# Kernel tuning notes

Hardware: AMD Instinct MI355X
Metric: run time of the kernel (lower is better)

The kernel has to match this reference:

```python
import jax, jax.numpy as jnp
import numpy as np

B, T, C, H = 128, 512, 256, 64  # batch, seq (<= BLOCK_SIZE=512), EMBED_SIZE, HEAD_SIZE


def setup_inputs() -> dict:
    key = jax.random.key(0)
    k0, k1, k2, k3 = jax.random.split(key, 4)
    # nn.Linear(C, H, bias=False) applies x @ W.T with W:[H,C]; we store the
    # transposed weight [C,H] so the math x @ W is identical.
    scale = 1.0 / np.sqrt(C)  # rough Linear-init scale, values only matter for testing
    return {
        "input_embeddings": jax.random.normal(k0, (B, T, C), dtype=jnp.float32),
        "Wq": jax.random.normal(k1, (C, H), dtype=jnp.float32) * scale,
        "Wk": jax.random.normal(k2, (C, H), dtype=jnp.float32) * scale,
        "Wv": jax.random.normal(k3, (C, H), dtype=jnp.float32) * scale,
    }


def reference(input_embeddings, Wq, Wk, Wv):
    x = input_embeddings
    t = x.shape[1]
    h = Wq.shape[1]
    q = jnp.einsum("btc,ch->bth", x, Wq)
    k = jnp.einsum("btc,ch->bth", x, Wk)
    v = jnp.einsum("btc,ch->bth", x, Wv)
    # QK^T / sqrt(H), causal mask, softmax  (faithful to masked_fill(-inf))
    sim = jnp.einsum("bth,bsh->bts", q, k) / jnp.sqrt(jnp.asarray(h, x.dtype))
    causal = jnp.tril(jnp.ones((t, t), dtype=bool))
    sim = jnp.where(causal, sim, -jnp.inf)
    wei = jax.nn.softmax(sim, axis=-1)
    out = jnp.einsum("bts,bsh->bth", wei, v)
    return out
```

## Files before the change

### kernel.cpp

```cpp
#include <hip/hip_runtime.h>
#include <hip/hip_bf16.h>
#include <math.h>

#define Bn 128
#define Tn 512
#define Cn 256
#define Hn 64
#define HP2 72
#define SCL 0.18033688011112042f

typedef __attribute__((ext_vector_type(8))) short short8v;
typedef __attribute__((ext_vector_type(4))) float float4v;

__device__ __forceinline__ ushort f2bf(float f) {
    __hip_bfloat16 h = __float2bfloat16(f);
    return *reinterpret_cast<ushort*>(&h);
}

__global__ __launch_bounds__(256) void prep_w_kernel(
    const float* __restrict__ Wq, const float* __restrict__ Wk,
    const float* __restrict__ Wv, ushort* __restrict__ wcT4)
{
    const int g   = blockIdx.x;
    const int nh  = g / 96;
    const int row = g % 96;
    const int c   = threadIdx.x;
    const int kc  = c >> 6;
    const int k2  = c & 63;
    const float* W;
    int h;
    if (row < 64) { W = nh ? Wk : Wq; h = row; }
    else          { W = Wv; h = nh * 32 + (row - 64); }
    wcT4[(((nh * 4 + kc) * 96) + row) * 64 + (k2 ^ ((row & 7) << 3))] =
        f2bf(W[c * Hn + h]);
}

__global__ __launch_bounds__(256) void qkv_mfma_kernel(
    const float* __restrict__ x, const ushort* __restrict__ wcT4,
    ushort* __restrict__ q, ushort* __restrict__ k, ushort* __restrict__ vT)
{
    __shared__ char lds[40960];
    const int WOFF = 16384;

    const int tid  = threadIdx.x;
    const int lane = tid & 63;
    const int wv   = tid >> 6;
    const int lr   = lane & 15;
    const int hi   = lane >> 4;
    const int wr   = wv >> 1;
    const int wc   = wv & 1;

    const int bid     = blockIdx.x;
    const int nh      = (bid >> 3) & 1;
    const int rowtile = (bid & 7) | ((bid >> 4) << 3);
    const long rows0  = (long)rowtile * 128;

    const char* gw = (const char*)wcT4 + (long)nh * 4 * 12288;
    const float4* x4 = (const float4*)x;

    #pragma unroll
    for (int i = 0; i < 3; ++i) {
        int off = (wv * 3 + i) * 1024;
        __builtin_amdgcn_global_load_lds(
            (const __attribute__((address_space(1))) unsigned int*)(gw + off + (lane << 4)),
            (__attribute__((address_space(3))) unsigned int*)(lds + WOFF + off),
            16, 0, 0);
    }
    float4 xr[8];
    #pragma unroll
    for (int i = 0; i < 8; ++i) {
        int idx = tid + i * 256;
        int r = idx >> 4, f = idx & 15;
        xr[i] = x4[(rows0 + r) * 64 + f];
    }

    float4v acc[4][3];
    #pragma unroll
    for (int s = 0; s < 4; ++s)
        #pragma unroll
        for (int n = 0; n < 3; ++n) acc[s][n] = (float4v){0.f, 0.f, 0.f, 0.f};

    for (int kc = 0; kc < 4; ++kc) {
        const int par = kc & 1;
        __syncthreads();

        #pragma unroll
        for (int i = 0; i < 8; ++i) {
            int idx = tid + i * 256;
            int r = idx >> 4, f = idx & 15;
            union { ushort u[4]; uint2 p; } pk;
            pk.u[0] = f2bf(xr[i].x); pk.u[1] = f2bf(xr[i].y);
            pk.u[2] = f2bf(xr[i].z); pk.u[3] = f2bf(xr[i].w);
            *(uint2*)(lds + r * 128 + ((f * 8) ^ ((r & 7) << 4))) = pk.p;
        }
        __syncthreads();

        if (kc < 3) {
            const char* gw2 = gw + (kc + 1) * 12288;
            #pragma unroll
            for (int i = 0; i < 3; ++i) {
                int off = (wv * 3 + i) * 1024;
                __builtin_amdgcn_global_load_lds(
                    (const __attribute__((address_space(1))) unsigned int*)(gw2 + off + (lane << 4)),
                    (__attribute__((address_space(3))) unsigned int*)(lds + WOFF + (1 - par) * 12288 + off),
                    16, 0, 0);
            }
            #pragma unroll
            for (int i = 0; i < 8; ++i) {
                int idx = tid + i * 256;
                int r = idx >> 4, f = idx & 15;
                xr[i] = x4[(rows0 + r) * 64 + (kc + 1) * 16 + f];
            }
        }

        const char* wb = lds + WOFF + par * 12288;
        #pragma unroll
        for (int ks = 0; ks < 2; ++ks) {
            const int kb = ks * 64 + hi * 16;
            short8v a[4];
            #pragma unroll
            for (int s = 0; s < 4; ++s) {
                int r = wr * 64 + s * 16 + lr;
                a[s] = *(const short8v*)(lds + r * 128 + (kb ^ ((r & 7) << 4)));
            }
            #pragma unroll
            for (int n = 0; n < 3; ++n) {
                int wrow = wc * 48 + n * 16 + lr;
                short8v wf = *(const short8v*)(wb + wrow * 128 + (kb ^ ((wrow & 7) << 4)));
                #pragma unroll
                for (int s = 0; s < 4; ++s)
                    acc[s][n] = __builtin_amdgcn_mfma_f32_16x16x32_bf16(a[s], wf, acc[s][n], 0, 0, 0);
            }
        }
    }

    __syncthreads();

    #pragma unroll
    for (int s = 0; s < 4; ++s) {
        const int tb = wr * 64 + s * 16 + hi * 4;
        #pragma unroll
        for (int n = 0; n < 3; ++n) {
            const int col16 = wc * 48 + n * 16;
            if (col16 < 64) {
                int h = col16 + lr;
                #pragma unroll
                for (int reg = 0; reg < 4; ++reg) {
                    int t = tb + reg;
                    *(ushort*)(lds + t * 128 + ((h * 2) ^ ((t & 7) << 4))) =
                        f2bf(acc[s][n][reg]);
                }
            } else {
                int hl = col16 - 64 + lr;
                ushort4 pk;
                pk.x = f2bf(acc[s][n][0]); pk.y = f2bf(acc[s][n][1]);
                pk.z = f2bf(acc[s][n][2]); pk.w = f2bf(acc[s][n][3]);
                *(ushort4*)(lds + WOFF + hl * 256 + ((tb * 2) ^ ((hl & 7) << 4))) = pk;
            }
        }
    }
    __syncthreads();

    {
        const int bb = (int)(rows0 >> 9);
        const int t0 = (int)(rows0 & 511);
        ushort* qk = nh ? k : q;
        #pragma unroll
        for (int i = 0; i < 4; ++i) {
            int idx = tid + i * 256;
            int t = idx >> 3, f = idx & 7;
            uint4 w = *(const uint4*)(lds + t * 128 + ((f * 16) ^ ((t & 7) << 4)));
            *(uint4*)(qk + (rows0 + t) * Hn + f * 8) = w;
        }
        #pragma unroll
        for (int i = 0; i < 2; ++i) {
            int idx = tid + i * 256;
            int hl = idx >> 4, fv = idx & 15;
            uint4 w = *(const uint4*)(lds + WOFF + hl * 256 + ((fv * 16) ^ ((hl & 7) << 4)));
            *(uint4*)(vT + ((long)bb * Hn + nh * 32 + hl) * Tn + t0 + fv * 8) = w;
        }
    }
}

__global__ __launch_bounds__(512) void attn_mfma_kernel(
    const ushort* __restrict__ q, const ushort* __restrict__ k,
    const ushort* __restrict__ vT, float* __restrict__ out)
{
    __shared__ ushort Ks[64 * HP2];
    __shared__ ushort Vt[64 * HP2];
    __shared__ ushort Pl[8][16 * HP2];

    const int tid = threadIdx.x;
    const int f   = blockIdx.x;
    const int c   = f & 255;
    const int b   = c >> 1;
    const int par = c & 1;
    const int qtp = (f < 256) ? par : (3 - par);
    const int ntiles = 2 * qtp + 2;

    const long base  = (long)b * Tn * Hn;
    const int lane = tid & 63;
    const int wv   = tid >> 6;
    const int lr   = lane & 15;
    const int hi   = lane >> 4;

    const int qrow_g = qtp * 128 + wv * 16;
    const int mrow0  = qrow_g + hi * 4;

    short8v qa[2];
    {
        const ushort* qp = q + base + (long)(qrow_g + lr) * Hn + hi * 8;
        qa[0] = *(const short8v*)(qp);
        qa[1] = *(const short8v*)(qp + 32);
    }

    const int sr  = tid >> 3;
    const int sc8 = tid & 7;
    uint4 kreg = *(const uint4*)(k + base + (long)sr * Hn + sc8 * 8);
    uint4 vreg = *(const uint4*)(vT + base + (long)sr * Tn + sc8 * 8);

    float4v o[4];
    #pragma unroll
    for (int n = 0; n < 4; ++n) o[n] = (float4v){0.f, 0.f, 0.f, 0.f};
    float m[4], l[4];
    #pragma unroll
    for (int reg = 0; reg < 4; ++reg) { m[reg] = -INFINITY; l[reg] = 0.f; }

    for (int kt = 0; kt < ntiles; ++kt) {
        __syncthreads();
        *(uint4*)&Ks[sr * HP2 + sc8 * 8] = kreg;
        *(uint4*)&Vt[sr * HP2 + sc8 * 8] = vreg;
        __syncthreads();
        if (kt + 1 < ntiles) {
            kreg = *(const uint4*)(k  + base + (long)((kt + 1) * 64 + sr) * Hn + sc8 * 8);
            vreg = *(const uint4*)(vT + base + (long)sr * Tn + (kt + 1) * 64 + sc8 * 8);
        }
        if (kt * 64 > qrow_g + 15) continue;

        float4v s4[4];
        #pragma unroll
        for (int n = 0; n < 4; ++n) s4[n] = (float4v){0.f, 0.f, 0.f, 0.f};
        #pragma unroll
        for (int ks = 0; ks < 2; ++ks) {
            short8v a = qa[ks];
            #pragma unroll
            for (int n = 0; n < 4; ++n) {
                short8v bb = *(const short8v*)&Ks[(n * 16 + lr) * HP2 + ks * 32 + hi * 8];
                s4[n] = __builtin_amdgcn_mfma_f32_16x16x32_bf16(a, bb, s4[n], 0, 0, 0);
            }
        }

        const bool partial = (kt * 64 + 63 > qrow_g);
        if (partial) {
            #pragma unroll
            for (int n = 0; n < 4; ++n) {
                int kcol = kt * 64 + n * 16 + lr;
                #pragma unroll
                for (int reg = 0; reg < 4; ++reg) {
                    float y = s4[n][reg] * SCL;
                    s4[n][reg] = (kcol <= mrow0 + reg) ? y : -INFINITY;
                }
            }
        } else {
            #pragma unroll
            for (int n = 0; n < 4; ++n)
                #pragma unroll
                for (int reg = 0; reg < 4; ++reg) s4[n][reg] *= SCL;
        }

        #pragma unroll
        for (int reg = 0; reg < 4; ++reg) {
            float mx = fmaxf(fmaxf(s4[0][reg], s4[1][reg]),
                             fmaxf(s4[2][reg], s4[3][reg]));
            mx = fmaxf(mx, __shfl_xor(mx, 1));
            mx = fmaxf(mx, __shfl_xor(mx, 2));
            mx = fmaxf(mx, __shfl_xor(mx, 4));
            mx = fmaxf(mx, __shfl_xor(mx, 8));
            float mN = fmaxf(m[reg], mx);
            float sc = exp2f(m[reg] - mN);
            float ps = 0.f;
            #pragma unroll
            for (int n = 0; n < 4; ++n) {
                float p = exp2f(s4[n][reg] - mN);
                s4[n][reg] = p;
                ps += p;
            }
            ps += __shfl_xor(ps, 1);
            ps += __shfl_xor(ps, 2);
            ps += __shfl_xor(ps, 4);
            ps += __shfl_xor(ps, 8);
            l[reg] = l[reg] * sc + ps;
            m[reg] = mN;
            #pragma unroll
            for (int n = 0; n < 4; ++n) o[n][reg] *= sc;
        }

        #pragma unroll
        for (int n = 0; n < 4; ++n)
            #pragma unroll
            for (int reg = 0; reg < 4; ++reg)
                Pl[wv][(hi * 4 + reg) * HP2 + n * 16 + lr] = f2bf(s4[n][reg]);

        #pragma unroll
        for (int ks = 0; ks < 2; ++ks) {
            short8v a = *(const short8v*)&Pl[wv][lr * HP2 + ks * 32 + hi * 8];
            #pragma unroll
            for (int n = 0; n < 4; ++n) {
                short8v bb = *(const short8v*)&Vt[(n * 16 + lr) * HP2 + ks * 32 + hi * 8];
                o[n] = __builtin_amdgcn_mfma_f32_16x16x32_bf16(a, bb, o[n], 0, 0, 0);
            }
        }
    }

    #pragma unroll
    for (int reg = 0; reg < 4; ++reg) {
        float inv = 1.0f / l[reg];
        float* orow = out + base + (long)(mrow0 + reg) * Hn;
        #pragma unroll
        for (int n = 0; n < 4; ++n)
            orow[n * 16 + lr] = o[n][reg] * inv;
    }
}

extern "C" void kernel_launch(void* const* d_in, const int* in_sizes, int n_in,
                              void* d_out, int out_size, void* d_ws, size_t ws_size,
                              hipStream_t stream) {
    const float* x  = (const float*)d_in[0];
    const float* Wq = (const float*)d_in[1];
    const float* Wk = (const float*)d_in[2];
    const float* Wv = (const float*)d_in[3];
    float* out = (float*)d_out;

    const size_t n = (size_t)Bn * Tn * Hn;
    ushort* qws  = (ushort*)d_ws;
    ushort* kws  = qws + n;
    ushort* vTs  = kws + n;
    ushort* wcT4 = vTs + n;

    prep_w_kernel<<<dim3(192), 256, 0, stream>>>(Wq, Wk, Wv, wcT4);
    qkv_mfma_kernel<<<dim3(1024), 256, 0, stream>>>(x, wcT4, qws, kws, vTs);
    attn_mfma_kernel<<<dim3(512), 512, 0, stream>>>(qws, kws, vTs, out);
}
```

Baseline: 49.41 us.

## Preload all QKV weight chunks into LDS and double-buffer x tiles

The QKV projection kernel now loads all four weight K-chunks into LDS up front with async global-to-LDS loads, instead of streaming them through a two-slot buffer. The x tile is double-buffered in both registers (xA/xB) and LDS, and hand-placed vmcnt waits plus lighter barrier clusters replace the per-iteration double __syncthreads. The goal is to cut barrier stalls and overlap global loads with MFMA work. The cost is LDS per block growing from 40KB to 80KB, which can lower blocks per CU, and the manual waitcnt values depend on the exact load issue order.

```diff
diff --git a/kernel.cpp b/kernel.cpp
--- a/kernel.cpp
+++ b/kernel.cpp
@@ -39,8 +39,8 @@
     const float* __restrict__ x, const ushort* __restrict__ wcT4,
     ushort* __restrict__ q, ushort* __restrict__ k, ushort* __restrict__ vT)
 {
-    __shared__ char lds[40960];
-    const int WOFF = 16384;
+    __shared__ char lds[81920];
+    const int XOFF = 49152;
 
     const int tid  = threadIdx.x;
     const int lane = tid & 63;
@@ -55,23 +55,71 @@
     const int rowtile = (bid & 7) | ((bid >> 4) << 3);
     const long rows0  = (long)rowtile * 128;
 
-    const char* gw = (const char*)wcT4 + (long)nh * 4 * 12288;
+    const char* gw = (const char*)wcT4 + (long)nh * 49152;
     const float4* x4 = (const float4*)x;
 
-    #pragma unroll
-    for (int i = 0; i < 3; ++i) {
-        int off = (wv * 3 + i) * 1024;
-        __builtin_amdgcn_global_load_lds(
-            (const __attribute__((address_space(1))) unsigned int*)(gw + off + (lane << 4)),
-            (__attribute__((address_space(3))) unsigned int*)(lds + WOFF + off),
-            16, 0, 0);
-    }
-    float4 xr[8];
-    #pragma unroll
-    for (int i = 0; i < 8; ++i) {
-        int idx = tid + i * 256;
-        int r = idx >> 4, f = idx & 15;
-        xr[i] = x4[(rows0 + r) * 64 + f];
+#define LOADX(dst, kc_) do {                                                  \
+    _Pragma("unroll")                                                         \
+    for (int i = 0; i < 8; ++i) {                                             \
+        int idx = tid + i * 256;                                              \
+        int r = idx >> 4, f = idx & 15;                                       \
+        dst[i] = x4[(rows0 + r) * 64 + (kc_) * 16 + f];                       \
+    } } while (0)
+
+#define STOREX(src, buf_) do {                                                \
+    char* xd = lds + XOFF + (buf_) * 16384;                                   \
+    _Pragma("unroll")                                                         \
+    for (int i = 0; i < 8; ++i) {                                             \
+        int idx = tid + i * 256;                                              \
+        int r = idx >> 4, f = idx & 15;                                       \
+        union { ushort u[4]; uint2 p; } pk;                                   \
+        pk.u[0] = f2bf(src[i].x); pk.u[1] = f2bf(src[i].y);                   \
+        pk.u[2] = f2bf(src[i].z); pk.u[3] = f2bf(src[i].w);                   \
+        *(uint2*)(xd + r * 128 + ((f * 8) ^ ((r & 7) << 4))) = pk.p;          \
+    } } while (0)
+
+#define MFMA_CHUNK(CH, BUF) do {                                              \
+    const char* wb  = lds + (CH) * 12288;                                     \
+    const char* xbf = lds + XOFF + (BUF) * 16384;                             \
+    _Pragma("unroll")                                                         \
+    for (int ks = 0; ks < 2; ++ks) {                                          \
+        const int kb = ks * 64 + hi * 16;                                     \
+        short8v a_[4];                                                        \
+        _Pragma("unroll")                                                     \
+        for (int s = 0; s < 4; ++s) {                                         \
+            int r = wr * 64 + s * 16 + lr;                                    \
+            a_[s] = *(const short8v*)(xbf + r * 128 + (kb ^ ((r & 7) << 4))); \
+        }                                                                     \
+        _Pragma("unroll")                                                     \
+        for (int n = 0; n < 3; ++n) {                                         \
+            int wrow = wc * 48 + n * 16 + lr;                                 \
+            short8v wf = *(const short8v*)(wb + wrow * 128 +                  \
+                                           (kb ^ ((wrow & 7) << 4)));         \
+            _Pragma("unroll")                                                 \
+            for (int s = 0; s < 4; ++s)                                       \
+                acc[s][n] = __builtin_amdgcn_mfma_f32_16x16x32_bf16(          \
+                    a_[s], wf, acc[s][n], 0, 0, 0);                           \
+        }                                                                     \
+    } } while (0)
+
+#define BAR_CLUSTER() do {                                                    \
+    asm volatile("s_waitcnt lgkmcnt(0)" ::: "memory");                        \
+    __builtin_amdgcn_s_barrier();                                             \
+    __builtin_amdgcn_sched_barrier(0); } while (0)
+
+    float4 xA[8], xB[8];
+    LOADX(xA, 0);
+    LOADX(xB, 1);
+    #pragma unroll
+    for (int c = 0; c < 4; ++c) {
+        #pragma unroll
+        for (int i = 0; i < 3; ++i) {
+            int off = c * 12288 + wv * 3072 + i * 1024;
+            __builtin_amdgcn_global_load_lds(
+                (const __attribute__((address_space(1))) unsigned int*)(gw + off + (lane << 4)),
+                (__attribute__((address_space(3))) unsigned int*)(lds + off),
+                16, 0, 0);
+        }
     }
 
     float4v acc[4][3];
@@ -80,59 +128,30 @@
         #pragma unroll
         for (int n = 0; n < 3; ++n) acc[s][n] = (float4v){0.f, 0.f, 0.f, 0.f};
 
-    for (int kc = 0; kc < 4; ++kc) {
-        const int par = kc & 1;
-        __syncthreads();
-
-        #pragma unroll
-        for (int i = 0; i < 8; ++i) {
-            int idx = tid + i * 256;
-            int r = idx >> 4, f = idx & 15;
-            union { ushort u[4]; uint2 p; } pk;
-            pk.u[0] = f2bf(xr[i].x); pk.u[1] = f2bf(xr[i].y);
-            pk.u[2] = f2bf(xr[i].z); pk.u[3] = f2bf(xr[i].w);
-            *(uint2*)(lds + r * 128 + ((f * 8) ^ ((r & 7) << 4))) = pk.p;
-        }
-        __syncthreads();
-
-        if (kc < 3) {
-            const char* gw2 = gw + (kc + 1) * 12288;
-            #pragma unroll
-            for (int i = 0; i < 3; ++i) {
-                int off = (wv * 3 + i) * 1024;
-                __builtin_amdgcn_global_load_lds(
-                    (const __attribute__((address_space(1))) unsigned int*)(gw2 + off + (lane << 4)),
-                    (__attribute__((address_space(3))) unsigned int*)(lds + WOFF + (1 - par) * 12288 + off),
-                    16, 0, 0);
-            }
-            #pragma unroll
-            for (int i = 0; i < 8; ++i) {
-                int idx = tid + i * 256;
-                int r = idx >> 4, f = idx & 15;
-                xr[i] = x4[(rows0 + r) * 64 + (kc + 1) * 16 + f];
-            }
-        }
-
-        const char* wb = lds + WOFF + par * 12288;
-        #pragma unroll
-        for (int ks = 0; ks < 2; ++ks) {
-            const int kb = ks * 64 + hi * 16;
-            short8v a[4];
-            #pragma unroll
-            for (int s = 0; s < 4; ++s) {
-                int r = wr * 64 + s * 16 + lr;
-                a[s] = *(const short8v*)(lds + r * 128 + (kb ^ ((r & 7) << 4)));
-            }
-            #pragma unroll
-            for (int n = 0; n < 3; ++n) {
-                int wrow = wc * 48 + n * 16 + lr;
-                short8v wf = *(const short8v*)(wb + wrow * 128 + (kb ^ ((wrow & 7) << 4)));
-                #pragma unroll
-                for (int s = 0; s < 4; ++s)
-                    acc[s][n] = __builtin_amdgcn_mfma_f32_16x16x32_bf16(a[s], wf, acc[s][n], 0, 0, 0);
-            }
-        }
-    }
+    STOREX(xA, 0);
+    LOADX(xA, 2);
+    asm volatile("s_waitcnt vmcnt(17)" ::: "memory");
+    BAR_CLUSTER();
+    MFMA_CHUNK(0, 0);
+
+    STOREX(xB, 1);
+    LOADX(xB, 3);
+    asm volatile("s_waitcnt vmcnt(22)" ::: "memory");
+    BAR_CLUSTER();
+    MFMA_CHUNK(1, 1);
+
+    STOREX(xA, 0);
+    BAR_CLUSTER();
+    MFMA_CHUNK(2, 0);
+
+    STOREX(xB, 1);
+    BAR_CLUSTER();
+    MFMA_CHUNK(3, 1);
+
+#undef LOADX
+#undef STOREX
+#undef MFMA_CHUNK
+#undef BAR_CLUSTER
 
     __syncthreads();
 
@@ -155,7 +174,7 @@
                 ushort4 pk;
                 pk.x = f2bf(acc[s][n][0]); pk.y = f2bf(acc[s][n][1]);
                 pk.z = f2bf(acc[s][n][2]); pk.w = f2bf(acc[s][n][3]);
-                *(ushort4*)(lds + WOFF + hl * 256 + ((tb * 2) ^ ((hl & 7) << 4))) = pk;
+                *(ushort4*)(lds + 65536 + hl * 256 + ((tb * 2) ^ ((hl & 7) << 4))) = pk;
             }
         }
     }
@@ -176,7 +195,7 @@
         for (int i = 0; i < 2; ++i) {
             int idx = tid + i * 256;
             int hl = idx >> 4, fv = idx & 15;
-            uint4 w = *(const uint4*)(lds + WOFF + hl * 256 + ((fv * 16) ^ ((hl & 7) << 4)));
+            uint4 w = *(const uint4*)(lds + 65536 + hl * 256 + ((fv * 16) ^ ((hl & 7) << 4)));
             *(uint4*)(vT + ((long)bb * Hn + nh * 32 + hl) * Tn + t0 + fv * 8) = w;
         }
     }
```

Result: slower. 50.75 us (+2.7%).
